# Kernel optimization log

Measured on AMD Instinct MI355X. Metric: run time of the kernel, lower is better.

Reference implementation:

```python
import jax, jax.numpy as jnp
import numpy as np

BATCH = 2048
INPUT_DIM = 256
NUM_SUBCARRIERS = 256
HIDDEN_DIM = 256


def setup_inputs() -> dict:
    key = jax.random.key(0)
    ks = jax.random.split(key, 7)
    C, I, H = NUM_SUBCARRIERS, INPUT_DIM, HIDDEN_DIM
    # PyTorch nn.Linear default init: U(-1/sqrt(fan_in), 1/sqrt(fan_in))
    s1 = 1.0 / np.sqrt(I)
    s2 = 1.0 / np.sqrt(H)
    x = jax.random.normal(ks[0], (BATCH, I), dtype=jnp.float32)
    W1 = jax.random.uniform(ks[1], (C, I, H), jnp.float32, -s1, s1)
    b1 = jax.random.uniform(ks[2], (C, H), jnp.float32, -s1, s1)
    W2 = jax.random.uniform(ks[3], (C, H, H), jnp.float32, -s2, s2)
    b2 = jax.random.uniform(ks[4], (C, H), jnp.float32, -s2, s2)
    W3 = jax.random.uniform(ks[5], (C, H), jnp.float32, -s2, s2)  # [C, H] (out dim 1 squeezed)
    b3 = jax.random.uniform(ks[6], (C,), jnp.float32, -s2, s2)
    return {"x": x, "W1": W1, "b1": b1, "W2": W2, "b2": b2, "W3": W3, "b3": b3}


def reference(x, W1, b1, W2, b2, W3, b3):
    # Stacked (batched) version of the per-subcarrier Python loop:
    # for each subcarrier c: relu(relu(x @ W1[c] + b1[c]) @ W2[c] + b2[c]) @ W3[c] + b3[c]
    h1 = jax.nn.relu(jnp.einsum('bi,cih->cbh', x, W1) + b1[:, None, :])   # [C, B, H]
    h2 = jax.nn.relu(jnp.einsum('cbh,chk->cbk', h1, W2) + b2[:, None, :])  # [C, B, H]
    out = jnp.einsum('cbh,ch->cb', h2, W3) + b3[:, None]                   # [C, B]
    return out.T  # [B, C], matches torch.cat(outputs, dim=1)
```

## Files before the change

### kernel.cpp

```cpp
#include <hip/hip_runtime.h>

typedef unsigned short u16;
using u16x4  = __attribute__((ext_vector_type(4))) unsigned short;
using u16x8  = __attribute__((ext_vector_type(8))) unsigned short;
using bf16x8 = __attribute__((ext_vector_type(8))) short;
using f32x4  = __attribute__((ext_vector_type(4))) float;
using f32x16 = __attribute__((ext_vector_type(16))) float;

__device__ __forceinline__ u16 f2bf(float f) {
  union { float f; unsigned u; } v; v.f = f;
  unsigned r = v.u + 0x7FFFu + ((v.u >> 16) & 1u);
  return (u16)(r >> 16);
}

__device__ __forceinline__ unsigned cvt_pk_bf16(float a, float b) {
  unsigned d;
  asm("v_cvt_pk_bf16_f32 %0, %1, %2" : "=v"(d) : "v"(a), "v"(b));
  return d;
}

__global__ __launch_bounds__(256) void prepass_k(
    const float* __restrict__ W1, const float* __restrict__ W2,
    u16* __restrict__ w1t, u16* __restrict__ w2t,
    const float* __restrict__ x, u16* __restrict__ xb) {
  const int bid = blockIdx.x;
  const int t = threadIdx.x;
  if (bid >= 8192) {
    int i = (bid - 8192) * 256 + t;
    float4 v = ((const float4*)x)[i];
    u16x4 u;
    u.x = f2bf(v.x); u.y = f2bf(v.y); u.z = f2bf(v.z); u.w = f2bf(v.w);
    ((u16x4*)xb)[i] = u;
    return;
  }
  const int mat = bid >> 4;
  const int ib  = bid & 15;
  const float* src = (mat < 256) ? (W1 + mat * 65536) : (W2 + (mat - 256) * 65536);
  u16*       dst   = (mat < 256) ? (w1t + mat * 65536) : (w2t + (mat - 256) * 65536);
  const int i0 = ib * 16;

  float r[16];
#pragma unroll
  for (int j = 0; j < 16; ++j)
    r[j] = src[(i0 + j) * 256 + t];

  uint4 lo, hi;
  lo.x = cvt_pk_bf16(r[0],  r[1]);  lo.y = cvt_pk_bf16(r[2],  r[3]);
  lo.z = cvt_pk_bf16(r[4],  r[5]);  lo.w = cvt_pk_bf16(r[6],  r[7]);
  hi.x = cvt_pk_bf16(r[8],  r[9]);  hi.y = cvt_pk_bf16(r[10], r[11]);
  hi.z = cvt_pk_bf16(r[12], r[13]); hi.w = cvt_pk_bf16(r[14], r[15]);
  u16* o = dst + ib * 4096 + t * 16;
  *(uint4*)(o)     = lo;
  *(uint4*)(o + 8) = hi;
}

__global__ __launch_bounds__(512, 4) void rf_main_k(
    const u16* __restrict__ xb, const u16* __restrict__ w1t, const u16* __restrict__ w2t,
    const float* __restrict__ b1, const float* __restrict__ b2,
    const float* __restrict__ w3, const float* __restrict__ b3,
    float* __restrict__ out) {
  __shared__ u16 sH[128 * 264];
  __shared__ float red[8 * 128];

  const int bid  = blockIdx.x;
  const int xcd  = bid & 7;
  const int j8   = bid >> 3;
  const int c    = xcd * 32 + (j8 >> 4);
  const int b0   = (j8 & 15) * 128;
  const int t    = threadIdx.x;
  const int lane = t & 63;
  const int w    = t >> 6;
  const int l31  = lane & 31;
  const int hi   = lane >> 5;
  const bool hiH = hi != 0;
  const int wq   = w & 3;
  const int bh   = w >> 2;
  const int m_base = wq * 64;
  const int n_base = bh * 64;

  const u16* w1c = w1t + c * 65536;
  const u16* w2c = w2t + c * 65536;
  const int aoff  = (m_base + l31) * 16 + hi * 8;
  const int bbase = (n_base + l31) * 264 + hi * 8;
  const int bidx  = __builtin_amdgcn_readfirstlane(c * 256 + m_base);

  f32x16 acc[2][2];
  bf16x8 aS[3][2];
  bf16x8 bS[2][2];

#define LOADA(dst, base)                                         \
  { dst[0] = *(const bf16x8*)(base);                             \
    dst[1] = *(const bf16x8*)((base) + 512); }

#define LOADB(dst, ch)                                           \
  { dst[0] = *(const bf16x8*)&sH[bbase + (ch) * 16];             \
    dst[1] = *(const bf16x8*)&sH[bbase + (ch) * 16 + 8448]; }

#define COMPUTE(afr, bfr)                                        \
  { __builtin_amdgcn_s_setprio(1);                               \
    acc[0][0] = __builtin_amdgcn_mfma_f32_32x32x16_bf16(afr[0], bfr[0], acc[0][0], 0, 0, 0); \
    acc[1][0] = __builtin_amdgcn_mfma_f32_32x32x16_bf16(afr[1], bfr[0], acc[1][0], 0, 0, 0); \
    acc[0][1] = __builtin_amdgcn_mfma_f32_32x32x16_bf16(afr[0], bfr[1], acc[0][1], 0, 0, 0); \
    acc[1][1] = __builtin_amdgcn_mfma_f32_32x32x16_bf16(afr[1], bfr[1], acc[1][1], 0, 0, 0); \
    __builtin_amdgcn_s_setprio(0); }

#define INIT_ACC(bp)                                             \
  { _Pragma("unroll")                                            \
    for (int _mi = 0; _mi < 2; ++_mi) {                          \
      _Pragma("unroll")                                          \
      for (int _g = 0; _g < 4; ++_g) {                           \
        f32x4 _lo = *(const f32x4*)((bp) + bidx + _mi * 32 + _g * 8);     \
        f32x4 _h4 = *(const f32x4*)((bp) + bidx + _mi * 32 + _g * 8 + 4); \
        _Pragma("unroll")                                        \
        for (int _r = 0; _r < 4; ++_r) {                         \
          float _v = hiH ? _h4[_r] : _lo[_r];                    \
          acc[_mi][0][_g * 4 + _r] = _v;                         \
          acc[_mi][1][_g * 4 + _r] = _v;                         \
        } } } }

  LOADA(aS[0], w1c + 0 * 4096 + aoff);
  LOADA(aS[1], w1c + 1 * 4096 + aoff);

#pragma unroll
  for (int i = 0; i < 8; ++i) {
    int flat = i * 512 + t;
    int r = flat >> 5, s = flat & 31;
    u16x8 g = *(const u16x8*)(xb + (b0 + r) * 256 + s * 8);
    *(u16x8*)&sH[r * 264 + s * 8] = g;
  }
  INIT_ACC(b1);
  __syncthreads();

  LOADB(bS[0], 0);
#pragma unroll
  for (int ch = 0; ch < 16; ++ch) {
    const u16* ab = (ch + 2 < 16) ? (w1c + (ch + 2) * 4096) : (w2c + (ch - 14) * 4096);
    LOADA(aS[(ch + 2) % 3], ab + aoff);
    if (ch + 1 < 16) LOADB(bS[(ch + 1) & 1], ch + 1);
    COMPUTE(aS[ch % 3], bS[ch & 1]);
  }

  __syncthreads();
#pragma unroll
  for (int mi = 0; mi < 2; ++mi)
#pragma unroll
    for (int nj = 0; nj < 2; ++nj) {
      const int row = n_base + nj * 32 + l31;
#pragma unroll
      for (int g = 0; g < 4; ++g) {
        float v0 = fmaxf(acc[mi][nj][g * 4 + 0], 0.f);
        float v1 = fmaxf(acc[mi][nj][g * 4 + 1], 0.f);
        float v2 = fmaxf(acc[mi][nj][g * 4 + 2], 0.f);
        float v3 = fmaxf(acc[mi][nj][g * 4 + 3], 0.f);
        uint2 p;
        p.x = cvt_pk_bf16(v0, v1);
        p.y = cvt_pk_bf16(v2, v3);
        *(uint2*)&sH[row * 264 + m_base + mi * 32 + g * 8 + 4 * hi] = p;
      }
    }
  INIT_ACC(b2);
  __syncthreads();

  LOADB(bS[0], 0);
#pragma unroll
  for (int ch = 0; ch < 16; ++ch) {
    if (ch + 2 < 16) LOADA(aS[ch % 3], w2c + (ch + 2) * 4096 + aoff);
    if (ch + 1 < 16) LOADB(bS[(ch + 1) & 1], ch + 1);
    COMPUTE(aS[(ch + 1) % 3], bS[ch & 1]);
  }

  float part0 = 0.f, part1 = 0.f;
#pragma unroll
  for (int mi = 0; mi < 2; ++mi)
#pragma unroll
    for (int g = 0; g < 4; ++g) {
      f32x4 wlo = *(const f32x4*)(w3 + bidx + mi * 32 + g * 8);
      f32x4 whi = *(const f32x4*)(w3 + bidx + mi * 32 + g * 8 + 4);
#pragma unroll
      for (int r = 0; r < 4; ++r) {
        float wv = hiH ? whi[r] : wlo[r];
        part0 += fmaxf(acc[mi][0][g * 4 + r], 0.f) * wv;
        part1 += fmaxf(acc[mi][1][g * 4 + r], 0.f) * wv;
      }
    }
  red[(wq * 2 + hi) * 128 + n_base + l31]      = part0;
  red[(wq * 2 + hi) * 128 + n_base + 32 + l31] = part1;
  __syncthreads();
  if (t < 128) {
    float v = b3[c];
#pragma unroll
    for (int k = 0; k < 8; ++k) v += red[k * 128 + t];
    out[(b0 + t) * 256 + c] = v;
  }
#undef LOADA
#undef LOADB
#undef COMPUTE
#undef INIT_ACC
}

extern "C" void kernel_launch(void* const* d_in, const int* in_sizes, int n_in,
                              void* d_out, int out_size, void* d_ws, size_t ws_size,
                              hipStream_t stream) {
  const float* x  = (const float*)d_in[0];
  const float* W1 = (const float*)d_in[1];
  const float* b1 = (const float*)d_in[2];
  const float* W2 = (const float*)d_in[3];
  const float* b2 = (const float*)d_in[4];
  const float* W3 = (const float*)d_in[5];
  const float* b3 = (const float*)d_in[6];
  float* out = (float*)d_out;

  char* ws = (char*)d_ws;
  u16* xb  = (u16*)ws;
  u16* w1t = (u16*)(ws + (1u << 20));
  u16* w2t = (u16*)(ws + (1u << 20) + (32u << 20));

  prepass_k <<<8704, 256, 0, stream>>>(W1, W2, w1t, w2t, x, xb);
  rf_main_k <<<4096, 512, 0, stream>>>(xb, w1t, w2t, b1, b2, W3, b3, out);
}
```

Baseline: 299.2 us.

## Halve batch tile per block and convert x to bf16 inside main kernel

The main kernel now uses 256-thread blocks covering 64 batch rows instead of 512 threads covering 128, doubling the grid to 8192 blocks. The per-block x tile is read as fp32 and converted to bf16 in-kernel, so the separate x conversion in the prepass and its workspace buffer are removed. The weight prepass loads now use nontemporal hints. Smaller batch tiles mean each subcarrier's bf16 weights are streamed from L2/HBM by twice as many blocks, raising weight traffic per output in exchange for more parallelism and less LDS per block.

```diff
diff --git a/kernel.cpp b/kernel.cpp
--- a/kernel.cpp
+++ b/kernel.cpp
@@ -7,12 +7,6 @@
 using f32x4  = __attribute__((ext_vector_type(4))) float;
 using f32x16 = __attribute__((ext_vector_type(16))) float;
 
-__device__ __forceinline__ u16 f2bf(float f) {
-  union { float f; unsigned u; } v; v.f = f;
-  unsigned r = v.u + 0x7FFFu + ((v.u >> 16) & 1u);
-  return (u16)(r >> 16);
-}
-
 __device__ __forceinline__ unsigned cvt_pk_bf16(float a, float b) {
   unsigned d;
   asm("v_cvt_pk_bf16_f32 %0, %1, %2" : "=v"(d) : "v"(a), "v"(b));
@@ -21,18 +15,9 @@
 
 __global__ __launch_bounds__(256) void prepass_k(
     const float* __restrict__ W1, const float* __restrict__ W2,
-    u16* __restrict__ w1t, u16* __restrict__ w2t,
-    const float* __restrict__ x, u16* __restrict__ xb) {
+    u16* __restrict__ w1t, u16* __restrict__ w2t) {
   const int bid = blockIdx.x;
   const int t = threadIdx.x;
-  if (bid >= 8192) {
-    int i = (bid - 8192) * 256 + t;
-    float4 v = ((const float4*)x)[i];
-    u16x4 u;
-    u.x = f2bf(v.x); u.y = f2bf(v.y); u.z = f2bf(v.z); u.w = f2bf(v.w);
-    ((u16x4*)xb)[i] = u;
-    return;
-  }
   const int mat = bid >> 4;
   const int ib  = bid & 15;
   const float* src = (mat < 256) ? (W1 + mat * 65536) : (W2 + (mat - 256) * 65536);
@@ -42,7 +27,7 @@
   float r[16];
 #pragma unroll
   for (int j = 0; j < 16; ++j)
-    r[j] = src[(i0 + j) * 256 + t];
+    r[j] = __builtin_nontemporal_load(src + (i0 + j) * 256 + t);
 
   uint4 lo, hi;
   lo.x = cvt_pk_bf16(r[0],  r[1]);  lo.y = cvt_pk_bf16(r[2],  r[3]);
@@ -54,34 +39,31 @@
   *(uint4*)(o + 8) = hi;
 }
 
-__global__ __launch_bounds__(512, 4) void rf_main_k(
-    const u16* __restrict__ xb, const u16* __restrict__ w1t, const u16* __restrict__ w2t,
+__global__ __launch_bounds__(256, 4) void rf_main_k(
+    const float* __restrict__ x, const u16* __restrict__ w1t, const u16* __restrict__ w2t,
     const float* __restrict__ b1, const float* __restrict__ b2,
     const float* __restrict__ w3, const float* __restrict__ b3,
     float* __restrict__ out) {
-  __shared__ u16 sH[128 * 264];
-  __shared__ float red[8 * 128];
+  __shared__ u16 sH[64 * 264];
+  __shared__ float red[8 * 64];
 
   const int bid  = blockIdx.x;
   const int xcd  = bid & 7;
   const int j8   = bid >> 3;
-  const int c    = xcd * 32 + (j8 >> 4);
-  const int b0   = (j8 & 15) * 128;
+  const int c    = xcd * 32 + (j8 >> 5);
+  const int b0   = (j8 & 31) * 64;
   const int t    = threadIdx.x;
   const int lane = t & 63;
-  const int w    = t >> 6;
+  const int wq   = t >> 6;
   const int l31  = lane & 31;
   const int hi   = lane >> 5;
   const bool hiH = hi != 0;
-  const int wq   = w & 3;
-  const int bh   = w >> 2;
   const int m_base = wq * 64;
-  const int n_base = bh * 64;
 
   const u16* w1c = w1t + c * 65536;
   const u16* w2c = w2t + c * 65536;
   const int aoff  = (m_base + l31) * 16 + hi * 8;
-  const int bbase = (n_base + l31) * 264 + hi * 8;
+  const int bbase = l31 * 264 + hi * 8;
   const int bidx  = __builtin_amdgcn_readfirstlane(c * 256 + m_base);
 
   f32x16 acc[2][2];
@@ -123,10 +105,15 @@
 
 #pragma unroll
   for (int i = 0; i < 8; ++i) {
-    int flat = i * 512 + t;
+    int flat = i * 256 + t;
     int r = flat >> 5, s = flat & 31;
-    u16x8 g = *(const u16x8*)(xb + (b0 + r) * 256 + s * 8);
-    *(u16x8*)&sH[r * 264 + s * 8] = g;
+    const float* xp = x + (b0 + r) * 256 + s * 8;
+    float4 f0 = *(const float4*)(xp);
+    float4 f1 = *(const float4*)(xp + 4);
+    uint4 p;
+    p.x = cvt_pk_bf16(f0.x, f0.y); p.y = cvt_pk_bf16(f0.z, f0.w);
+    p.z = cvt_pk_bf16(f1.x, f1.y); p.w = cvt_pk_bf16(f1.z, f1.w);
+    *(uint4*)&sH[r * 264 + s * 8] = p;
   }
   INIT_ACC(b1);
   __syncthreads();
@@ -145,7 +132,7 @@
   for (int mi = 0; mi < 2; ++mi)
 #pragma unroll
     for (int nj = 0; nj < 2; ++nj) {
-      const int row = n_base + nj * 32 + l31;
+      const int row = nj * 32 + l31;
 #pragma unroll
       for (int g = 0; g < 4; ++g) {
         float v0 = fmaxf(acc[mi][nj][g * 4 + 0], 0.f);
@@ -183,13 +170,13 @@
         part1 += fmaxf(acc[mi][1][g * 4 + r], 0.f) * wv;
       }
     }
-  red[(wq * 2 + hi) * 128 + n_base + l31]      = part0;
-  red[(wq * 2 + hi) * 128 + n_base + 32 + l31] = part1;
-  __syncthreads();
-  if (t < 128) {
+  red[(wq * 2 + hi) * 64 + l31]      = part0;
+  red[(wq * 2 + hi) * 64 + 32 + l31] = part1;
+  __syncthreads();
+  if (t < 64) {
     float v = b3[c];
 #pragma unroll
-    for (int k = 0; k < 8; ++k) v += red[k * 128 + t];
+    for (int k = 0; k < 8; ++k) v += red[k * 64 + t];
     out[(b0 + t) * 256 + c] = v;
   }
 #undef LOADA
@@ -211,10 +198,9 @@
   float* out = (float*)d_out;
 
   char* ws = (char*)d_ws;
-  u16* xb  = (u16*)ws;
-  u16* w1t = (u16*)(ws + (1u << 20));
-  u16* w2t = (u16*)(ws + (1u << 20) + (32u << 20));
-
-  prepass_k <<<8704, 256, 0, stream>>>(W1, W2, w1t, w2t, x, xb);
-  rf_main_k <<<4096, 512, 0, stream>>>(xb, w1t, w2t, b1, b2, W3, b3, out);
-}
+  u16* w1t = (u16*)ws;
+  u16* w2t = (u16*)(ws + (32u << 20));
+
+  prepass_k <<<8192, 256, 0, stream>>>(W1, W2, w1t, w2t);
+  rf_main_k <<<8192, 256, 0, stream>>>(x, w1t, w2t, b1, b2, W3, b3, out);
+}
```

New measurement: 299.7 us. No clear change (+0.2%).
